# Performance work log

Hardware: AMD Instinct MI355X
Metric: run time of the kernel (lower is better)

The kernel has to match this reference:

```python
import jax, jax.numpy as jnp
import numpy as np
import math

EPS = 1e-7
N, M, K, D_IN, D_OUT = 8192, 32, 8, 64, 64
KP_EXTENT = 0.66

# ---- Lorentz manifold (curvature k = 1) helpers ----

def l_inner(x, y):
    # Lorentzian inner product, keepdim on last axis
    return -x[..., :1] * y[..., :1] + jnp.sum(x[..., 1:] * y[..., 1:], axis=-1, keepdims=True)

def l_dist(x, y):
    alpha = jnp.clip(-l_inner(x, y), 1.0 + EPS, None)
    return jnp.arccosh(alpha)[..., 0]

def expmap0(u):
    # u: tangent at origin, time component ignored-by-construction (zero)
    sp = u[..., 1:]
    un = jnp.sqrt(jnp.clip(jnp.sum(sp * sp, axis=-1, keepdims=True), 1e-14, None))
    return jnp.concatenate([jnp.cosh(un), jnp.sinh(un) * sp / un], axis=-1)

def expmap(x, u):
    un = jnp.sqrt(jnp.clip(l_inner(u, u), 1e-14, None))
    return jnp.cosh(un) * x + jnp.sinh(un) * u / un

def logmap(x, y):
    alpha = jnp.clip(-l_inner(x, y), 1.0 + EPS, None)
    d = jnp.arccosh(alpha)
    nom = y - alpha * x
    den = jnp.sqrt(jnp.clip(alpha * alpha - 1.0, 1e-14, None))
    return d * nom / den

def ptransp(x, y, v):
    # parallel transport of v from x to y
    return v + l_inner(y, v) / (1.0 - l_inner(x, y)) * (x + y)

def norm_midpoint(ave):
    den = jnp.sqrt(jnp.clip(jnp.abs(l_inner(ave, ave)), 1e-8, None))
    return ave / den


def setup_inputs() -> dict:
    key = jax.random.key(0)
    k1, k2, k3, k4, k5, k6 = jax.random.split(key, 6)
    # points on the hyperboloid: time = sqrt(1 + ||space||^2)
    sp = jax.random.normal(k1, (N, D_IN - 1), dtype=jnp.float32) * 0.5
    t = jnp.sqrt(1.0 + jnp.sum(sp * sp, axis=-1, keepdims=True))
    x = jnp.concatenate([t, sp], axis=-1)
    nei = jax.random.randint(k2, (N, M), 0, N, dtype=jnp.int32)
    nei_mask = jax.random.randint(k3, (N, M), 0, 2, dtype=jnp.int32)
    # kernel points: tangent vectors at origin (time comp 0), first point = center
    kp_sp = jax.random.normal(k4, (K, D_IN - 1), dtype=jnp.float32)
    kp_sp = kp_sp / jnp.linalg.norm(kp_sp, axis=-1, keepdims=True)
    radii = jax.random.uniform(k5, (K, 1), dtype=jnp.float32) * KP_EXTENT
    kp_sp = kp_sp * radii
    kp_sp = kp_sp.at[0].set(0.0)
    kernel_points = jnp.concatenate([jnp.zeros((K, 1), jnp.float32), kp_sp], axis=-1)
    # K LorentzLinear params
    stdv = 1.0 / math.sqrt(D_OUT)
    W = jax.random.uniform(k6, (K, D_OUT, D_IN), dtype=jnp.float32, minval=-stdv, maxval=stdv)
    W = W.at[:, :, 0].set(0.0)  # reset_parameters zeros first input column
    b = jnp.zeros((K, D_OUT), dtype=jnp.float32)
    scale = jnp.full((K,), math.log(10.0), dtype=jnp.float32)
    return {"x": x, "nei": nei, "nei_mask": nei_mask, "W": W, "b": b,
            "scale": scale, "kernel_points": kernel_points}


def reference(x, nei, nei_mask, W, b, scale, kernel_points):
    n, d = x.shape
    x_nei = x[nei]                      # [n, m, d] gather
    xr = x[:, None, :]                  # [n, 1, d]
    og_row = jnp.zeros((d,), x.dtype).at[0].set(1.0)
    # transport_x: map each neighborhood to the origin's tangent frame
    v = logmap(xr, x_nei)
    x0_nei = expmap0(ptransp(xr, og_row[None, None, :], v))   # [n, m, d]
    # kernel positions at the origin (transp=True => base point is origin)
    tmp = expmap(og_row[None, :], ptransp(og_row[None, :], og_row[None, :], kernel_points[1:]))
    x_kernel = jnp.concatenate([tmp, og_row[None, :]], axis=0)  # [K, d]
    # geodesic distances neighbor <-> kernel point: [n, K, m]
    dis = l_dist(x0_nei[:, None, :, :], x_kernel[None, :, None, :])
    dis = dis * nei_mask[:, None, :].astype(x.dtype)
    # K LorentzLinear transforms (vectorized over K): [n, K, m, d_out]
    h = jnp.einsum('nmd,kod->nkmo', x0_nei, W) + b[None, :, None, :]
    time = jax.nn.sigmoid(h[..., :1]) * jnp.exp(scale)[None, :, None, None] + 1.0001
    nar = h[..., 1:]
    s = (time * time - 1.0) / jnp.clip(jnp.sum(nar * nar, axis=-1, keepdims=True), 1e-8, None)
    xt = jnp.concatenate([time, nar * jnp.sqrt(s)], axis=-1)
    # weighted Lorentz midpoint over kernel points, per neighbor: [n, m, d_out]
    per_nei = norm_midpoint(jnp.einsum('nkm,nkmo->nmo', dis, xt))
    # unweighted Lorentz midpoint over neighbors: [n, d_out]
    return norm_midpoint(per_nei.mean(axis=1))
```

## Files before the change

### kernel.cpp

```cpp
#include <hip/hip_runtime.h>
#include <hip/hip_bf16.h>

#define N_NODES 8192
#define M_NEI   32
#define K_PTS   8
#define D       64
#define EPS_    1e-7f

typedef float f4v __attribute__((ext_vector_type(4)));
typedef short s8v __attribute__((ext_vector_type(8)));

__device__ __forceinline__ ushort f2bf(float f) {
  __hip_bfloat16 h = __float2bfloat16(f);
  return *reinterpret_cast<ushort*>(&h);
}
__device__ __forceinline__ float bf2f(ushort u) {
  __hip_bfloat16 h;
  *reinterpret_cast<ushort*>(&h) = u;
  return __bfloat162float(h);
}
__device__ __forceinline__ float frcp(float x)  { return __builtin_amdgcn_rcpf(x); }
__device__ __forceinline__ float frsq(float x)  { return __builtin_amdgcn_rsqf(x); }
__device__ __forceinline__ float fsqrt(float x) { return __builtin_amdgcn_sqrtf(x); }
__device__ __forceinline__ float facosh(float a) {
  float den = fsqrt(fmaxf(a * a - 1.f, 1e-14f));
  return __logf(a + den);
}

__global__ void prep_xk(const float* __restrict__ kp, float* __restrict__ xk) {
  int d = threadIdx.x;
  for (int kk = 0; kk < K_PTS - 1; ++kk) {
    float v = kp[(kk + 1) * D + d];
    float p = (d == 0) ? 0.f : v * v;
    #pragma unroll
    for (int s = 1; s < 64; s <<= 1) p += __shfl_xor(p, s);
    float un = sqrtf(fmaxf(p, 1e-14f));
    float sh = sinhf(un) / un;
    xk[kk * D + d] = (d == 0) ? coshf(un) : sh * v;
  }
  xk[(K_PTS - 1) * D + d] = (d == 0) ? 1.f : 0.f;
}

__global__ void prep_wb(const float* __restrict__ W, ushort* __restrict__ WF) {
  int idx = blockIdx.x * 256 + threadIdx.x;
  int k    = idx >> 9;
  int ct   = (idx >> 7) & 3;
  int ks   = (idx >> 6) & 1;
  int lane = idx & 63;
  int o  = ct * 16 + (lane & 15);
  int db = (lane >> 4) * 8 + ks * 32;
  const float* wrow = W + (k * 64 + o) * 64 + db;
  s8v hi, lo;
  #pragma unroll
  for (int j = 0; j < 8; ++j) {
    float w = wrow[j];
    ushort h = f2bf(w);
    hi[j] = (short)h;
    lo[j] = (short)f2bf(w - bf2f(h));
  }
  int f = (k * 4 + ct) * 2 + ks;
  *(s8v*)(WF + (size_t)(f * 2 + 0) * 512 + lane * 8) = hi;
  *(s8v*)(WF + (size_t)(f * 2 + 1) * 512 + lane * 8) = lo;
}

__launch_bounds__(256, 3)
__global__ void kpa_main(const float* __restrict__ x, const int* __restrict__ nei,
                         const int* __restrict__ mask, const ushort* __restrict__ WF,
                         const float* __restrict__ b, const float* __restrict__ scale,
                         const float* __restrict__ xk, float* __restrict__ out) {
  __shared__ __align__(16) float  xr_s[D];
  __shared__ __align__(16) float  xk_s[K_PTS * D];
  __shared__ __align__(16) ushort Ah_lds[M_NEI * D];
  __shared__ __align__(16) ushort Al_lds[M_NEI * D];
  __shared__ float dis_s[K_PTS * 33];
  __shared__ __align__(16) float  red_w[4][M_NEI * 68];
  __shared__ __align__(16) float  redp[4 * D];

  const int n  = blockIdx.x;
  const int t  = threadIdx.x;
  const int w4 = t >> 6;
  const int l  = t & 63;
  const int cl = l & 15;
  const int gr = l >> 4;

  if (t < D) xr_s[t] = x[n * D + t];
  xk_s[t] = xk[t]; xk_s[t + 256] = xk[t + 256];
  __syncthreads();

  {
    const int m  = t >> 3;
    const int l8 = t & 7;
    const int d0 = l8 * 8;
    const int ni = nei[n * M_NEI + m];
    float y[8], xr[8];
    {
      float4 ya = *(const float4*)(x + ni * D + d0);
      float4 yb = *(const float4*)(x + ni * D + d0 + 4);
      y[0]=ya.x; y[1]=ya.y; y[2]=ya.z; y[3]=ya.w;
      y[4]=yb.x; y[5]=yb.y; y[6]=yb.z; y[7]=yb.w;
      float4 ra = *(const float4*)(xr_s + d0);
      float4 rb = *(const float4*)(xr_s + d0 + 4);
      xr[0]=ra.x; xr[1]=ra.y; xr[2]=ra.z; xr[3]=ra.w;
      xr[4]=rb.x; xr[5]=rb.y; xr[6]=rb.z; xr[7]=rb.w;
    }
    float p = 0.f;
    #pragma unroll
    for (int j = 0; j < 8; ++j) p += xr[j] * y[j];
    if (l8 == 0) p -= 2.f * xr[0] * y[0];
    p += __shfl_xor(p, 1); p += __shfl_xor(p, 2); p += __shfl_xor(p, 4);
    float alpha = fmaxf(-p, 1.f + EPS_);
    float den = fsqrt(fmaxf(alpha * alpha - 1.f, 1e-14f));
    float dd  = __logf(alpha + den);
    float f   = dd * frcp(den);
    float v[8];
    #pragma unroll
    for (int j = 0; j < 8; ++j) v[j] = f * (y[j] - alpha * xr[j]);
    float v0 = __shfl(v[0], l & 56);
    float c  = -v0 * frcp(1.f + xr_s[0]);
    float wv[8];
    float q = 0.f;
    #pragma unroll
    for (int j = 0; j < 8; ++j) { wv[j] = v[j] + c * xr[j]; q += wv[j] * wv[j]; }
    if (l8 == 0) q -= wv[0] * wv[0];
    q += __shfl_xor(q, 1); q += __shfl_xor(q, 2); q += __shfl_xor(q, 4);
    float un = fsqrt(fmaxf(q, 1e-14f));
    float e  = __expf(un);
    float ei = frcp(e);
    float sh = (0.5f * (e - ei)) * frcp(un);
    float x0v[8];
    #pragma unroll
    for (int j = 0; j < 8; ++j) x0v[j] = sh * wv[j];
    if (l8 == 0) x0v[0] = 0.5f * (e + ei);
    {
      s8v hi, lo;
      #pragma unroll
      for (int j = 0; j < 8; ++j) {
        uint u = __float_as_uint(x0v[j]);
        hi[j] = (short)(ushort)(u >> 16);
        float lof = x0v[j] - __uint_as_float(u & 0xffff0000u);
        uint ul = __float_as_uint(lof);
        lo[j] = (short)(ushort)((ul + 0x7fffu + ((ul >> 16) & 1u)) >> 16);
      }
      int byte = m * 128 + d0 * 2;
      int swz  = byte ^ ((m & 7) << 4);
      *(s8v*)((char*)Ah_lds + swz) = hi;
      *(s8v*)((char*)Al_lds + swz) = lo;
    }
    float msk = (float)mask[n * M_NEI + m];
    #pragma unroll
    for (int kk = 0; kk < K_PTS; ++kk) {
      float pp = 0.f;
      #pragma unroll
      for (int j = 0; j < 8; ++j) pp += x0v[j] * xk_s[kk * D + d0 + j];
      if (l8 == 0) pp -= 2.f * x0v[0] * xk_s[kk * D];
      pp += __shfl_xor(pp, 1); pp += __shfl_xor(pp, 2); pp += __shfl_xor(pp, 4);
      float al = fmaxf(-pp, 1.f + EPS_);
      float dk = facosh(al) * msk;
      if (l8 == kk) dis_s[kk * 33 + m] = dk;
    }
  }
  __syncthreads();

  float yacc[2][4][4];
  #pragma unroll
  for (int rt = 0; rt < 2; ++rt)
    #pragma unroll
    for (int r = 0; r < 4; ++r)
      #pragma unroll
      for (int ct = 0; ct < 4; ++ct) yacc[rt][r][ct] = 0.f;

  #pragma unroll
  for (int p = 0; p < 2; ++p) {
    const int k = w4 + p * 4;
    s8v bh[4][2], bl[4][2];
    #pragma unroll
    for (int ct = 0; ct < 4; ++ct)
      #pragma unroll
      for (int ks = 0; ks < 2; ++ks) {
        int f = (k * 4 + ct) * 2 + ks;
        bh[ct][ks] = *(const s8v*)(WF + (size_t)(f * 2 + 0) * 512 + l * 8);
        bl[ct][ks] = *(const s8v*)(WF + (size_t)(f * 2 + 1) * 512 + l * 8);
      }
    f4v acc[4][2];
    #pragma unroll
    for (int ct = 0; ct < 4; ++ct)
      #pragma unroll
      for (int rt = 0; rt < 2; ++rt)
        acc[ct][rt] = (f4v){0.f, 0.f, 0.f, 0.f};

    #pragma unroll
    for (int rt = 0; rt < 2; ++rt) {
      const int row = cl + rt * 16;
      s8v ah[2], al_[2];
      #pragma unroll
      for (int ks = 0; ks < 2; ++ks) {
        int byte = row * 128 + (gr * 8 + ks * 32) * 2;
        int swz  = byte ^ ((row & 7) << 4);
        ah[ks]  = *(const s8v*)((const char*)Ah_lds + swz);
        al_[ks] = *(const s8v*)((const char*)Al_lds + swz);
      }
      #pragma unroll
      for (int ct = 0; ct < 4; ++ct)
        #pragma unroll
        for (int ks = 0; ks < 2; ++ks) {
          acc[ct][rt] = __builtin_amdgcn_mfma_f32_16x16x32_bf16(ah[ks],  bh[ct][ks], acc[ct][rt], 0, 0, 0);
          acc[ct][rt] = __builtin_amdgcn_mfma_f32_16x16x32_bf16(ah[ks],  bl[ct][ks], acc[ct][rt], 0, 0, 0);
          acc[ct][rt] = __builtin_amdgcn_mfma_f32_16x16x32_bf16(al_[ks], bh[ct][ks], acc[ct][rt], 0, 0, 0);
        }
    }

    float bv[4];
    #pragma unroll
    for (int ct = 0; ct < 4; ++ct) bv[ct] = b[k * 64 + ct * 16 + cl];
    #pragma unroll
    for (int ct = 0; ct < 4; ++ct)
      #pragma unroll
      for (int rt = 0; rt < 2; ++rt)
        #pragma unroll
        for (int r = 0; r < 4; ++r) acc[ct][rt][r] += bv[ct];

    const float es = __expf(scale[k]);
    #pragma unroll
    for (int rt = 0; rt < 2; ++rt)
      #pragma unroll
      for (int r = 0; r < 4; ++r) {
        const int m = rt * 16 + gr * 4 + r;
        float h0 = __shfl(acc[0][rt][r], l & 48);
        float ss = acc[0][rt][r]*acc[0][rt][r] + acc[1][rt][r]*acc[1][rt][r]
                 + acc[2][rt][r]*acc[2][rt][r] + acc[3][rt][r]*acc[3][rt][r];
        ss += __shfl_xor(ss, 1); ss += __shfl_xor(ss, 2);
        ss += __shfl_xor(ss, 4); ss += __shfl_xor(ss, 8);
        float nar2 = fmaxf(ss - h0 * h0, 1e-8f);
        float time = es * frcp(1.f + __expf(-h0)) + 1.0001f;
        float sq   = fsqrt(time * time - 1.f) * frsq(nar2);
        float dm   = dis_s[k * 33 + m];
        float dmsq = dm * sq;
        yacc[rt][r][0] += (cl == 0) ? dm * time : dmsq * acc[0][rt][r];
        yacc[rt][r][1] += dmsq * acc[1][rt][r];
        yacc[rt][r][2] += dmsq * acc[2][rt][r];
        yacc[rt][r][3] += dmsq * acc[3][rt][r];
      }
  }
  #pragma unroll
  for (int rt = 0; rt < 2; ++rt)
    #pragma unroll
    for (int r = 0; r < 4; ++r) {
      const int m = rt * 16 + gr * 4 + r;
      float* rw = &red_w[w4][m * 68];
      rw[cl]      = yacc[rt][r][0];
      rw[16 + cl] = yacc[rt][r][1];
      rw[32 + cl] = yacc[rt][r][2];
      rw[48 + cl] = yacc[rt][r][3];
    }
  __syncthreads();

  {
    const int m  = t >> 3;
    const int l8 = t & 7;
    const int o0 = l8 * 8;
    f4v s0 = (f4v){0.f,0.f,0.f,0.f}, s1 = s0;
    #pragma unroll
    for (int w = 0; w < 4; ++w) {
      s0 += *(const f4v*)&red_w[w][m * 68 + o0];
      s1 += *(const f4v*)&red_w[w][m * 68 + o0 + 4];
    }
    float v[8] = {s0.x, s0.y, s0.z, s0.w, s1.x, s1.y, s1.z, s1.w};
    float ip = 0.f;
    #pragma unroll
    for (int j = 0; j < 8; ++j) ip += v[j] * v[j];
    if (l8 == 0) ip -= 2.f * v[0] * v[0];
    ip += __shfl_xor(ip, 1); ip += __shfl_xor(ip, 2); ip += __shfl_xor(ip, 4);
    float rin = frsq(fmaxf(fabsf(ip), 1e-8f));
    #pragma unroll
    for (int j = 0; j < 8; ++j) {
      float z = v[j] * rin;
      z += __shfl_xor(z, 8); z += __shfl_xor(z, 16); z += __shfl_xor(z, 32);
      v[j] = z;
    }
    if (l < 8) {
      #pragma unroll
      for (int j = 0; j < 8; ++j) redp[w4 * D + l8 * 8 + j] = v[j];
    }
  }
  __syncthreads();
  if (t < D) {
    float mv = (redp[t] + redp[D + t] + redp[2 * D + t] + redp[3 * D + t]) * (1.f / 32.f);
    float ip = (t == 0) ? -mv * mv : mv * mv;
    #pragma unroll
    for (int s2 = 1; s2 < 64; s2 <<= 1) ip += __shfl_xor(ip, s2);
    out[n * D + t] = mv * frsq(fmaxf(fabsf(ip), 1e-8f));
  }
}

extern "C" void kernel_launch(void* const* d_in, const int* in_sizes, int n_in,
                              void* d_out, int out_size, void* d_ws, size_t ws_size,
                              hipStream_t stream) {
  const float* x     = (const float*)d_in[0];
  const int*   nei   = (const int*)d_in[1];
  const int*   mask  = (const int*)d_in[2];
  const float* W     = (const float*)d_in[3];
  const float* b     = (const float*)d_in[4];
  const float* scale = (const float*)d_in[5];
  const float* kp    = (const float*)d_in[6];
  float* out = (float*)d_out;

  ushort* WF = (ushort*)d_ws;
  float*  xk = (float*)(WF + 65536);

  prep_wb<<<16, 256, 0, stream>>>(W, WF);
  prep_xk<<<1, 64, 0, stream>>>(kp, xk);
  kpa_main<<<N_NODES, 256, 0, stream>>>(x, nei, mask, WF, b, scale, xk, out);
}
```

Before: 124.5 us.

## Repartition MFMA work so each wave owns a row tile and four kernel points

Each wave now handles one 16-row tile of neighbors and four kernel points in a rolled loop, instead of all 32 rows and two kernel points. This shrinks the per-wave accumulator and weight-fragment register footprint, so launch bounds rise to 4 blocks per SM and the cross-wave LDS reduction buffer halves. The acosh for distances is now computed once per lane rather than inside the kernel-point loop. The cost is that each wave reloads its weight fragments per kernel point without register reuse across two row tiles, and the rolled loop may expose global load latency.

```diff
diff --git a/kernel.cpp b/kernel.cpp
--- a/kernel.cpp
+++ b/kernel.cpp
@@ -63,7 +63,7 @@
   *(s8v*)(WF + (size_t)(f * 2 + 1) * 512 + lane * 8) = lo;
 }
 
-__launch_bounds__(256, 3)
+__launch_bounds__(256, 4)
 __global__ void kpa_main(const float* __restrict__ x, const int* __restrict__ nei,
                          const int* __restrict__ mask, const ushort* __restrict__ WF,
                          const float* __restrict__ b, const float* __restrict__ scale,
@@ -73,7 +73,7 @@
   __shared__ __align__(16) ushort Ah_lds[M_NEI * D];
   __shared__ __align__(16) ushort Al_lds[M_NEI * D];
   __shared__ float dis_s[K_PTS * 33];
-  __shared__ __align__(16) float  red_w[4][M_NEI * 68];
+  __shared__ __align__(16) float  red_w[2][M_NEI * 68];
   __shared__ __align__(16) float  redp[4 * D];
 
   const int n  = blockIdx.x;
@@ -82,6 +82,8 @@
   const int l  = t & 63;
   const int cl = l & 15;
   const int gr = l >> 4;
+  const int wm = w4 & 1;
+  const int wk = w4 >> 1;
 
   if (t < D) xr_s[t] = x[n * D + t];
   xk_s[t] = xk[t]; xk_s[t + 256] = xk[t + 256];
@@ -147,6 +149,7 @@
       *(s8v*)((char*)Al_lds + swz) = lo;
     }
     float msk = (float)mask[n * M_NEI + m];
+    float mypp = 0.f;
     #pragma unroll
     for (int kk = 0; kk < K_PTS; ++kk) {
       float pp = 0.f;
@@ -154,116 +157,88 @@
       for (int j = 0; j < 8; ++j) pp += x0v[j] * xk_s[kk * D + d0 + j];
       if (l8 == 0) pp -= 2.f * x0v[0] * xk_s[kk * D];
       pp += __shfl_xor(pp, 1); pp += __shfl_xor(pp, 2); pp += __shfl_xor(pp, 4);
-      float al = fmaxf(-pp, 1.f + EPS_);
-      float dk = facosh(al) * msk;
-      if (l8 == kk) dis_s[kk * 33 + m] = dk;
-    }
-  }
-  __syncthreads();
-
-  float yacc[2][4][4];
-  #pragma unroll
-  for (int rt = 0; rt < 2; ++rt)
-    #pragma unroll
-    for (int r = 0; r < 4; ++r)
-      #pragma unroll
-      for (int ct = 0; ct < 4; ++ct) yacc[rt][r][ct] = 0.f;
-
-  #pragma unroll
-  for (int p = 0; p < 2; ++p) {
-    const int k = w4 + p * 4;
-    s8v bh[4][2], bl[4][2];
-    #pragma unroll
-    for (int ct = 0; ct < 4; ++ct)
+      mypp = (l8 == kk) ? pp : mypp;
+    }
+    float al_ = fmaxf(-mypp, 1.f + EPS_);
+    dis_s[l8 * 33 + m] = facosh(al_) * msk;
+  }
+  __syncthreads();
+
+  const int row = wm * 16 + cl;
+  s8v ah[2], alo[2];
+  #pragma unroll
+  for (int ks = 0; ks < 2; ++ks) {
+    int byte = row * 128 + (gr * 8 + ks * 32) * 2;
+    int swz  = byte ^ ((row & 7) << 4);
+    ah[ks]  = *(const s8v*)((const char*)Ah_lds + swz);
+    alo[ks] = *(const s8v*)((const char*)Al_lds + swz);
+  }
+
+  float yacc[4][4];
+  #pragma unroll
+  for (int r = 0; r < 4; ++r)
+    #pragma unroll
+    for (int ct = 0; ct < 4; ++ct) yacc[r][ct] = 0.f;
+
+  for (int kq = 0; kq < 4; ++kq) {
+    const int k = wk * 4 + kq;
+    f4v acc[4];
+    #pragma unroll
+    for (int ct = 0; ct < 4; ++ct) {
+      acc[ct] = (f4v){0.f, 0.f, 0.f, 0.f};
       #pragma unroll
       for (int ks = 0; ks < 2; ++ks) {
         int f = (k * 4 + ct) * 2 + ks;
-        bh[ct][ks] = *(const s8v*)(WF + (size_t)(f * 2 + 0) * 512 + l * 8);
-        bl[ct][ks] = *(const s8v*)(WF + (size_t)(f * 2 + 1) * 512 + l * 8);
+        s8v bh = *(const s8v*)(WF + (size_t)(f * 2 + 0) * 512 + l * 8);
+        s8v bl = *(const s8v*)(WF + (size_t)(f * 2 + 1) * 512 + l * 8);
+        acc[ct] = __builtin_amdgcn_mfma_f32_16x16x32_bf16(ah[ks],  bh, acc[ct], 0, 0, 0);
+        acc[ct] = __builtin_amdgcn_mfma_f32_16x16x32_bf16(ah[ks],  bl, acc[ct], 0, 0, 0);
+        acc[ct] = __builtin_amdgcn_mfma_f32_16x16x32_bf16(alo[ks], bh, acc[ct], 0, 0, 0);
       }
-    f4v acc[4][2];
-    #pragma unroll
-    for (int ct = 0; ct < 4; ++ct)
-      #pragma unroll
-      for (int rt = 0; rt < 2; ++rt)
-        acc[ct][rt] = (f4v){0.f, 0.f, 0.f, 0.f};
-
-    #pragma unroll
-    for (int rt = 0; rt < 2; ++rt) {
-      const int row = cl + rt * 16;
-      s8v ah[2], al_[2];
-      #pragma unroll
-      for (int ks = 0; ks < 2; ++ks) {
-        int byte = row * 128 + (gr * 8 + ks * 32) * 2;
-        int swz  = byte ^ ((row & 7) << 4);
-        ah[ks]  = *(const s8v*)((const char*)Ah_lds + swz);
-        al_[ks] = *(const s8v*)((const char*)Al_lds + swz);
-      }
-      #pragma unroll
-      for (int ct = 0; ct < 4; ++ct)
-        #pragma unroll
-        for (int ks = 0; ks < 2; ++ks) {
-          acc[ct][rt] = __builtin_amdgcn_mfma_f32_16x16x32_bf16(ah[ks],  bh[ct][ks], acc[ct][rt], 0, 0, 0);
-          acc[ct][rt] = __builtin_amdgcn_mfma_f32_16x16x32_bf16(ah[ks],  bl[ct][ks], acc[ct][rt], 0, 0, 0);
-          acc[ct][rt] = __builtin_amdgcn_mfma_f32_16x16x32_bf16(al_[ks], bh[ct][ks], acc[ct][rt], 0, 0, 0);
-        }
-    }
-
-    float bv[4];
-    #pragma unroll
-    for (int ct = 0; ct < 4; ++ct) bv[ct] = b[k * 64 + ct * 16 + cl];
-    #pragma unroll
-    for (int ct = 0; ct < 4; ++ct)
-      #pragma unroll
-      for (int rt = 0; rt < 2; ++rt)
-        #pragma unroll
-        for (int r = 0; r < 4; ++r) acc[ct][rt][r] += bv[ct];
-
+    }
+    #pragma unroll
+    for (int ct = 0; ct < 4; ++ct) {
+      float bv = b[k * 64 + ct * 16 + cl];
+      #pragma unroll
+      for (int r = 0; r < 4; ++r) acc[ct][r] += bv;
+    }
     const float es = __expf(scale[k]);
     #pragma unroll
-    for (int rt = 0; rt < 2; ++rt)
-      #pragma unroll
-      for (int r = 0; r < 4; ++r) {
-        const int m = rt * 16 + gr * 4 + r;
-        float h0 = __shfl(acc[0][rt][r], l & 48);
-        float ss = acc[0][rt][r]*acc[0][rt][r] + acc[1][rt][r]*acc[1][rt][r]
-                 + acc[2][rt][r]*acc[2][rt][r] + acc[3][rt][r]*acc[3][rt][r];
-        ss += __shfl_xor(ss, 1); ss += __shfl_xor(ss, 2);
-        ss += __shfl_xor(ss, 4); ss += __shfl_xor(ss, 8);
-        float nar2 = fmaxf(ss - h0 * h0, 1e-8f);
-        float time = es * frcp(1.f + __expf(-h0)) + 1.0001f;
-        float sq   = fsqrt(time * time - 1.f) * frsq(nar2);
-        float dm   = dis_s[k * 33 + m];
-        float dmsq = dm * sq;
-        yacc[rt][r][0] += (cl == 0) ? dm * time : dmsq * acc[0][rt][r];
-        yacc[rt][r][1] += dmsq * acc[1][rt][r];
-        yacc[rt][r][2] += dmsq * acc[2][rt][r];
-        yacc[rt][r][3] += dmsq * acc[3][rt][r];
-      }
-  }
-  #pragma unroll
-  for (int rt = 0; rt < 2; ++rt)
-    #pragma unroll
     for (int r = 0; r < 4; ++r) {
-      const int m = rt * 16 + gr * 4 + r;
-      float* rw = &red_w[w4][m * 68];
-      rw[cl]      = yacc[rt][r][0];
-      rw[16 + cl] = yacc[rt][r][1];
-      rw[32 + cl] = yacc[rt][r][2];
-      rw[48 + cl] = yacc[rt][r][3];
-    }
+      const int m = wm * 16 + gr * 4 + r;
+      float h0 = __shfl(acc[0][r], l & 48);
+      float ss = acc[0][r]*acc[0][r] + acc[1][r]*acc[1][r]
+               + acc[2][r]*acc[2][r] + acc[3][r]*acc[3][r];
+      ss += __shfl_xor(ss, 1); ss += __shfl_xor(ss, 2);
+      ss += __shfl_xor(ss, 4); ss += __shfl_xor(ss, 8);
+      float nar2 = fmaxf(ss - h0 * h0, 1e-8f);
+      float time = es * frcp(1.f + __expf(-h0)) + 1.0001f;
+      float sq   = fsqrt(time * time - 1.f) * frsq(nar2);
+      float dm   = dis_s[k * 33 + m];
+      float dmsq = dm * sq;
+      yacc[r][0] += (cl == 0) ? dm * time : dmsq * acc[0][r];
+      yacc[r][1] += dmsq * acc[1][r];
+      yacc[r][2] += dmsq * acc[2][r];
+      yacc[r][3] += dmsq * acc[3][r];
+    }
+  }
+  #pragma unroll
+  for (int r = 0; r < 4; ++r) {
+    const int m = wm * 16 + gr * 4 + r;
+    float* rw = &red_w[wk][m * 68];
+    rw[cl]      = yacc[r][0];
+    rw[16 + cl] = yacc[r][1];
+    rw[32 + cl] = yacc[r][2];
+    rw[48 + cl] = yacc[r][3];
+  }
   __syncthreads();
 
   {
     const int m  = t >> 3;
     const int l8 = t & 7;
     const int o0 = l8 * 8;
-    f4v s0 = (f4v){0.f,0.f,0.f,0.f}, s1 = s0;
-    #pragma unroll
-    for (int w = 0; w < 4; ++w) {
-      s0 += *(const f4v*)&red_w[w][m * 68 + o0];
-      s1 += *(const f4v*)&red_w[w][m * 68 + o0 + 4];
-    }
+    f4v s0 = *(const f4v*)&red_w[0][m * 68 + o0]     + *(const f4v*)&red_w[1][m * 68 + o0];
+    f4v s1 = *(const f4v*)&red_w[0][m * 68 + o0 + 4] + *(const f4v*)&red_w[1][m * 68 + o0 + 4];
     float v[8] = {s0.x, s0.y, s0.z, s0.w, s1.x, s1.y, s1.z, s1.w};
     float ip = 0.f;
     #pragma unroll
```

New measurement: 126.5 us. About the same (+1.6%).
